# Optimization experiments

Hardware: AMD Instinct MI355X
Metric: run time of the kernel (lower is better)

Reference implementation:

```python
import jax, jax.numpy as jnp
import numpy as np

PIXEL_THRESHOLD = 0.4
FRACTION_THRESHOLD = 0.03
NUM_CLASSES = 20  # cls_idx in [0, 20)
N, H, W = 100, 640, 1280


def setup_inputs() -> dict:
    key = jax.random.key(0)
    k1, k2, k3 = jax.random.split(key, 3)
    cls_prob = jax.random.uniform(k1, (N,), dtype=jnp.float32)
    mask_prob = jax.random.normal(k2, (N, H, W), dtype=jnp.float32)
    cls_idx = jax.random.randint(k3, (N,), 0, NUM_CLASSES, dtype=jnp.int32)
    return {"cls_prob": cls_prob, "mask_prob": mask_prob, "cls_idx": cls_idx}


def reference(cls_prob, mask_prob, cls_idx):
    """Greedy confidence-sorted panoptic mask merging (mask_removal).

    Returns:
      keep:       [N] bool  - whether each (sorted) instance was kept
      kept_masks: [N,H,W]   - assigned raw mask probs (zeros where suppressed/unassigned)
      order:      [N] int   - descending-confidence permutation applied
    """
    # Sort by class confidence, descending (matches np.argsort(...)[::-1])
    order = jnp.argsort(cls_prob)[::-1]
    mp_raw = mask_prob[order]                      # [N,H,W] pre-softmax copy
    mp_soft = jax.nn.softmax(mp_raw, axis=0)       # softmax across instances per pixel
    ci = cls_idx[order]                            # [N]

    h, w = mp_raw.shape[-2:]
    pan0 = jnp.zeros((h, w), dtype=mp_raw.dtype)            # panoptic_image
    mimg0 = jnp.zeros((NUM_CLASSES + 1, h, w), dtype=mp_raw.dtype)  # per-class mask_image

    def step(carry, inp):
        pan, mimg = carry
        prob_s, prob_raw, cidx = inp
        logit = (prob_s >= PIXEL_THRESHOLD).astype(prob_s.dtype)  # binarized mask
        mask_sum = logit.sum()
        curr = mimg[cidx]                                         # [H,W]
        overlap_cnt = ((curr >= 1) & (logit == 1)).sum().astype(prob_s.dtype)
        overlap = overlap_cnt / jnp.maximum(mask_sum, 1.0)
        trivial = logit.max() == logit.min()  # all-zero or all-one mask
        keep = (~trivial) & (mask_sum > 0) & (overlap <= FRACTION_THRESHOLD)
        assign = (pan == 0) & (logit == 1) & keep                 # unclaimed pixels
        kept_mask = jnp.where(assign, prob_raw, 0.0)
        pan = jnp.where(assign, 1.0, pan)
        mimg = mimg.at[cidx].add(jnp.where(assign, logit, 0.0))
        return (pan, mimg), (keep, kept_mask)

    (_, _), (keep, kept_masks) = jax.lax.scan(step, (pan0, mimg0), (mp_soft, mp_raw, ci))
    return keep, kept_masks, order
```

## Files before the change

### kernel.cpp

```cpp
#include <hip/hip_runtime.h>

#define N_INST 100
#define HW_PIX 819200
#define NPAIR (N_INST * N_INST)

struct alignas(16) Ent { int p; int ab; float ra; float rb; };

__global__ __launch_bounds__(128) void k0_sort(
    const float* __restrict__ cls_prob,
    const int* __restrict__ cls_idx,
    int* __restrict__ order,
    int* __restrict__ cls_sorted,
    float* __restrict__ out_order) {
  __shared__ float v[N_INST];
  __shared__ int ordl[N_INST];
  int t = threadIdx.x;
  if (t < N_INST) v[t] = cls_prob[t];
  __syncthreads();
  if (t < N_INST) {
    float mv = v[t];
    int r = 0;
    for (int j = 0; j < N_INST; ++j) {
      float vj = v[j];
      r += (vj > mv) || (vj == mv && j > t);
    }
    ordl[r] = t;
  }
  __syncthreads();
  if (t < N_INST) {
    int o = ordl[t];
    order[t] = o;
    cls_sorted[t] = cls_idx[o];
    out_order[t] = (float)o;
  }
}

__global__ __launch_bounds__(256) void k1_cand(
    const float* __restrict__ mp,
    const int* __restrict__ order,
    unsigned int* __restrict__ masksum,
    unsigned int* __restrict__ paircnt,
    unsigned int* __restrict__ nc,
    Ent* __restrict__ list) {
  int p = blockIdx.x * 256 + threadIdx.x;
  float x[N_INST];
#pragma unroll
  for (int k = 0; k < N_INST; ++k)
    x[k] = mp[(size_t)order[k] * HW_PIX + p];
  float m = x[0];
#pragma unroll
  for (int k = 1; k < N_INST; ++k) m = fmaxf(m, x[k]);
  float denom = 0.0f, e1 = -1.0f, e2 = -1.0f, r1 = 0.0f, r2 = 0.0f;
  int s1 = 0, s2 = 0;
#pragma unroll
  for (int k = 0; k < N_INST; ++k) {
    float e = expf(x[k] - m);
    denom += e;
    if (e > e1)      { e2 = e1; s2 = s1; r2 = r1; e1 = e; s1 = k; r1 = x[k]; }
    else if (e > e2) { e2 = e;  s2 = k;  r2 = x[k]; }
  }
  bool c1 = (e1 / denom) >= 0.4f;
  bool c2 = (e2 / denom) >= 0.4f;
  if (c1) {
    int a = s1, b = 255;
    float ra = r1, rb = 0.0f;
    atomicAdd(&masksum[s1], 1u);
    if (c2) {
      atomicAdd(&masksum[s2], 1u);
      if (s2 < s1) { a = s2; ra = r2; b = s1; rb = r1; }
      else         { b = s2; rb = r2; }
      atomicAdd(&paircnt[a * N_INST + b], 1u);
    }
    unsigned idx = atomicAdd(nc, 1u);
    Ent e; e.p = p; e.ab = a | (b << 8); e.ra = ra; e.rb = rb;
    list[idx] = e;
  }
}

__global__ __launch_bounds__(256) void k2_keep(
    const unsigned int* __restrict__ paircnt,
    const unsigned int* __restrict__ masksum,
    const int* __restrict__ cls_sorted,
    unsigned long long* __restrict__ keepmask,
    float* __restrict__ out_keep) {
  __shared__ unsigned int pl[NPAIR];
  __shared__ unsigned int ms[N_INST];
  __shared__ int cl[N_INST];
  for (int i = threadIdx.x; i < NPAIR; i += 256) pl[i] = paircnt[i];
  if (threadIdx.x < N_INST) {
    ms[threadIdx.x] = masksum[threadIdx.x];
    cl[threadIdx.x] = cls_sorted[threadIdx.x];
  }
  __syncthreads();
  if (threadIdx.x < 64) {
    int l = threadIdx.x;
    int j2 = l + 64;
    int cA = cl[l];
    int cB = (j2 < N_INST) ? cl[j2] : -1;
    bool kA = false, kB = false;
    unsigned long long km0 = 0, km1 = 0;
    for (int s = 0; s < N_INST; ++s) {
      int cs = cl[s];
      unsigned int ov = 0;
      if (l < s && kA && cA == cs) ov += pl[l * N_INST + s];
      if (j2 < s && kB && cB == cs) ov += pl[j2 * N_INST + s];
#pragma unroll
      for (int off = 32; off >= 1; off >>= 1) ov += __shfl_xor((int)ov, off);
      unsigned int m_s = ms[s];
      float overlap = (float)ov / fmaxf((float)m_s, 1.0f);
      bool keep = (m_s > 0u) && (m_s < (unsigned)HW_PIX) && (overlap <= 0.03f);
      if (keep) { if (s < 64) km0 |= 1ull << s; else km1 |= 1ull << (s - 64); }
      if (s == l)  kA = keep;
      if (s == j2) kB = keep;
    }
    if (l == 0) { keepmask[0] = km0; keepmask[1] = km1; }
    out_keep[l] = kA ? 1.0f : 0.0f;
    if (j2 < N_INST) out_keep[j2] = kB ? 1.0f : 0.0f;
  }
}

__global__ __launch_bounds__(256) void k3_scatter(
    const unsigned int* __restrict__ nc,
    const Ent* __restrict__ list,
    const unsigned long long* __restrict__ keepmask,
    float* __restrict__ out_masks) {
  unsigned long long km0 = keepmask[0], km1 = keepmask[1];
  unsigned n = *nc;
  for (unsigned i = blockIdx.x * 256 + threadIdx.x; i < n; i += gridDim.x * 256) {
    Ent e = list[i];
    int a = e.ab & 0xFF;
    int b = (e.ab >> 8) & 0xFF;
    bool ka = (a < 64) ? (((km0 >> a) & 1ull) != 0)
                       : ((a < N_INST) && (((km1 >> (a - 64)) & 1ull) != 0));
    bool kb = (b < 64) ? (((km0 >> b) & 1ull) != 0)
                       : ((b < N_INST) && (((km1 >> (b - 64)) & 1ull) != 0));
    if (ka)      out_masks[(size_t)a * HW_PIX + e.p] = e.ra;
    else if (kb) out_masks[(size_t)b * HW_PIX + e.p] = e.rb;
  }
}

extern "C" void kernel_launch(void* const* d_in, const int* in_sizes, int n_in,
                              void* d_out, int out_size, void* d_ws, size_t ws_size,
                              hipStream_t stream) {
  const float* cls_prob = (const float*)d_in[0];
  const float* mp       = (const float*)d_in[1];
  const int*   cls_idx  = (const int*)d_in[2];
  float* out = (float*)d_out;

  char* ws = (char*)d_ws;
  int* order                   = (int*)(ws + 0);
  int* cls_sorted              = (int*)(ws + 400);
  unsigned long long* keepmask = (unsigned long long*)(ws + 800);
  unsigned int* nc             = (unsigned int*)(ws + 1024);
  unsigned int* masksum        = (unsigned int*)(ws + 2048);
  unsigned int* paircnt        = (unsigned int*)(ws + 4096);
  Ent* list                    = (Ent*)(ws + 65536);

  float* out_keep  = out;
  float* out_masks = out + N_INST;
  float* out_order = out + N_INST + (size_t)N_INST * HW_PIX;

  hipMemsetAsync(ws + 1024, 0, 4096 - 1024 + 40000, stream);
  hipMemsetAsync(out_masks, 0, (size_t)N_INST * HW_PIX * sizeof(float), stream);

  k0_sort<<<1, 128, 0, stream>>>(cls_prob, cls_idx, order, cls_sorted, out_order);
  k1_cand<<<HW_PIX / 256, 256, 0, stream>>>(mp, order, masksum, paircnt, nc, list);
  k2_keep<<<1, 256, 0, stream>>>(paircnt, masksum, cls_sorted, keepmask, out_keep);
  k3_scatter<<<128, 256, 0, stream>>>(nc, list, keepmask, out_masks);
}
```

Before: 611.1 us.

## Fuse output zeroing into candidate pass with vectorized online softmax and exact fallback

Drops both hipMemsetAsync calls. k0_sort now zeroes the counters and pair table, and k1_cand zero-fills the output masks while it streams the inputs. k1_cand handles four pixels per thread with float4 loads and an online max/denominator, which removes the 100-element register array. Only pixels whose softmax denominator is at or below 2.51, the only ones where the top probability can reach 0.4, go through an exact rescan that re-reads the inputs. The risks are __expf rounding near the guard threshold and the extra reads for the rare candidate pixels.

```diff
diff --git a/kernel.cpp b/kernel.cpp
--- a/kernel.cpp
+++ b/kernel.cpp
@@ -11,10 +11,17 @@
     const int* __restrict__ cls_idx,
     int* __restrict__ order,
     int* __restrict__ cls_sorted,
-    float* __restrict__ out_order) {
+    float* __restrict__ out_order,
+    unsigned int* __restrict__ nc,
+    unsigned int* __restrict__ masksum,
+    unsigned int* __restrict__ paircnt) {
+  int t = threadIdx.x;
+  if (t == 0) *nc = 0u;
+  for (int i = t; i < N_INST; i += 128) masksum[i] = 0u;
+  for (int i = t; i < NPAIR; i += 128) paircnt[i] = 0u;
+
   __shared__ float v[N_INST];
   __shared__ int ordl[N_INST];
-  int t = threadIdx.x;
   if (t < N_INST) v[t] = cls_prob[t];
   __syncthreads();
   if (t < N_INST) {
@@ -35,29 +42,22 @@
   }
 }
 
-__global__ __launch_bounds__(256) void k1_cand(
+__device__ __forceinline__ void exact_pixel(
+    int p, float m,
     const float* __restrict__ mp,
     const int* __restrict__ order,
     unsigned int* __restrict__ masksum,
     unsigned int* __restrict__ paircnt,
     unsigned int* __restrict__ nc,
     Ent* __restrict__ list) {
-  int p = blockIdx.x * 256 + threadIdx.x;
-  float x[N_INST];
-#pragma unroll
-  for (int k = 0; k < N_INST; ++k)
-    x[k] = mp[(size_t)order[k] * HW_PIX + p];
-  float m = x[0];
-#pragma unroll
-  for (int k = 1; k < N_INST; ++k) m = fmaxf(m, x[k]);
   float denom = 0.0f, e1 = -1.0f, e2 = -1.0f, r1 = 0.0f, r2 = 0.0f;
   int s1 = 0, s2 = 0;
-#pragma unroll
   for (int k = 0; k < N_INST; ++k) {
-    float e = expf(x[k] - m);
+    float xv = mp[(size_t)order[k] * HW_PIX + p];
+    float e = expf(xv - m);
     denom += e;
-    if (e > e1)      { e2 = e1; s2 = s1; r2 = r1; e1 = e; s1 = k; r1 = x[k]; }
-    else if (e > e2) { e2 = e;  s2 = k;  r2 = x[k]; }
+    if (e > e1)      { e2 = e1; s2 = s1; r2 = r1; e1 = e; s1 = k; r1 = xv; }
+    else if (e > e2) { e2 = e;  s2 = k;  r2 = xv; }
   }
   bool c1 = (e1 / denom) >= 0.4f;
   bool c2 = (e2 / denom) >= 0.4f;
@@ -74,6 +74,39 @@
     unsigned idx = atomicAdd(nc, 1u);
     Ent e; e.p = p; e.ab = a | (b << 8); e.ra = ra; e.rb = rb;
     list[idx] = e;
+  }
+}
+
+__global__ __launch_bounds__(256) void k1_cand(
+    const float* __restrict__ mp,
+    const int* __restrict__ order,
+    unsigned int* __restrict__ masksum,
+    unsigned int* __restrict__ paircnt,
+    unsigned int* __restrict__ nc,
+    Ent* __restrict__ list,
+    float* __restrict__ out_masks) {
+  const int p0 = (blockIdx.x * 256 + threadIdx.x) * 4;
+  float4 mx = make_float4(-INFINITY, -INFINITY, -INFINITY, -INFINITY);
+  float4 dn = make_float4(0.0f, 0.0f, 0.0f, 0.0f);
+  const float4 z = make_float4(0.0f, 0.0f, 0.0f, 0.0f);
+#pragma unroll
+  for (int k = 0; k < N_INST; ++k) {
+    const float4 x = *reinterpret_cast<const float4*>(
+        &mp[(size_t)order[k] * HW_PIX + p0]);
+    *reinterpret_cast<float4*>(&out_masks[(size_t)k * HW_PIX + p0]) = z;
+    float nm;
+    nm = fmaxf(mx.x, x.x); dn.x = dn.x * __expf(mx.x - nm) + __expf(x.x - nm); mx.x = nm;
+    nm = fmaxf(mx.y, x.y); dn.y = dn.y * __expf(mx.y - nm) + __expf(x.y - nm); mx.y = nm;
+    nm = fmaxf(mx.z, x.z); dn.z = dn.z * __expf(mx.z - nm) + __expf(x.z - nm); mx.z = nm;
+    nm = fmaxf(mx.w, x.w); dn.w = dn.w * __expf(mx.w - nm) + __expf(x.w - nm); mx.w = nm;
+  }
+  const float GUARD = 2.51f;
+  bool any = (dn.x <= GUARD) | (dn.y <= GUARD) | (dn.z <= GUARD) | (dn.w <= GUARD);
+  if (__builtin_expect(any, 0)) {
+    if (dn.x <= GUARD) exact_pixel(p0 + 0, mx.x, mp, order, masksum, paircnt, nc, list);
+    if (dn.y <= GUARD) exact_pixel(p0 + 1, mx.y, mp, order, masksum, paircnt, nc, list);
+    if (dn.z <= GUARD) exact_pixel(p0 + 2, mx.z, mp, order, masksum, paircnt, nc, list);
+    if (dn.w <= GUARD) exact_pixel(p0 + 3, mx.w, mp, order, masksum, paircnt, nc, list);
   }
 }
 
@@ -160,11 +193,10 @@
   float* out_masks = out + N_INST;
   float* out_order = out + N_INST + (size_t)N_INST * HW_PIX;
 
-  hipMemsetAsync(ws + 1024, 0, 4096 - 1024 + 40000, stream);
-  hipMemsetAsync(out_masks, 0, (size_t)N_INST * HW_PIX * sizeof(float), stream);
-
-  k0_sort<<<1, 128, 0, stream>>>(cls_prob, cls_idx, order, cls_sorted, out_order);
-  k1_cand<<<HW_PIX / 256, 256, 0, stream>>>(mp, order, masksum, paircnt, nc, list);
+  k0_sort<<<1, 128, 0, stream>>>(cls_prob, cls_idx, order, cls_sorted, out_order,
+                                 nc, masksum, paircnt);
+  k1_cand<<<HW_PIX / 1024, 256, 0, stream>>>(mp, order, masksum, paircnt, nc,
+                                             list, out_masks);
   k2_keep<<<1, 256, 0, stream>>>(paircnt, masksum, cls_sorted, keepmask, out_keep);
   k3_scatter<<<128, 256, 0, stream>>>(nc, list, keepmask, out_masks);
 }
```

Result: slower. 686.8 us (+12.4%).
